# Optimization experiments

Measured on AMD Instinct MI355X. Metric: run time of the kernel, lower is better.

Reference implementation:

```python
import jax, jax.numpy as jnp
import numpy as np
import math

N_EMBD = 2048
N_HEAD = 16
HEAD_DIM = N_EMBD // N_HEAD
EPS = 1e-6

def rms_norm(x, w):
    xf = x.astype(jnp.float32)
    n = xf * jax.lax.rsqrt(jnp.mean(xf * xf, axis=-1, keepdims=True) + EPS)
    return n.astype(x.dtype) * w

def rotate_embeddings(x):
    # pairs (a, b) -> (-b, a), interleaved on last dim
    x2 = x.reshape(*x.shape[:-1], -1, 2)
    rot = jnp.stack([-x2[..., 1], x2[..., 0]], axis=-1)
    return rot.reshape(x.shape)

def rope_angles(T, hd, dtype):
    # pos = 10000 ** ((-2*arange(0, hd, 2) - 1) / hd)  (faithful to source)
    i = jnp.arange(0, hd, 2, dtype=jnp.float32)
    pos = jnp.power(10000.0, (-2.0 * i - 1.0) / hd)
    token_seq = jnp.arange(T, dtype=jnp.float32)[:, None] * pos[None, :]  # [T, hd/2]
    ang = jnp.concatenate([token_seq, token_seq], axis=-1)  # [T, hd]
    return ang.astype(dtype)

def setup_inputs() -> dict:
    key = jax.random.key(0)
    k1, k2, k3 = jax.random.split(key, 3)
    B, T, C = 2, 2048, N_EMBD
    x = jax.random.normal(k1, (B, T, C), dtype=jnp.float32)
    s = 1.0 / math.sqrt(C)
    W_qkv = jax.random.normal(k2, (3 * C, C), dtype=jnp.float32) * s
    W_proj = jax.random.normal(k3, (C, C), dtype=jnp.float32) * s
    g_qk = jnp.ones((C,), dtype=jnp.float32)
    return {"x": x, "W_qkv": W_qkv, "W_proj": W_proj, "g_qk": g_qk}

def reference(x, W_qkv, W_proj, g_qk):
    B, T, C = x.shape
    H, hd = N_HEAD, HEAD_DIM
    qkv = x @ W_qkv.T  # [B, T, 3C]
    q, k, v = jnp.split(qkv, 3, axis=-1)
    q = rms_norm(q, g_qk)
    k = rms_norm(k, g_qk)
    # [B, H, T, hd]
    q = q.reshape(B, T, H, hd).transpose(0, 2, 1, 3)
    k = k.reshape(B, T, H, hd).transpose(0, 2, 1, 3)
    v = v.reshape(B, T, H, hd).transpose(0, 2, 1, 3)
    ang = rope_angles(T, hd, x.dtype)  # [T, hd]
    cos, sin = jnp.cos(ang), jnp.sin(ang)
    q = q * cos + rotate_embeddings(q) * sin
    k = k * cos + rotate_embeddings(k) * sin
    scale = 1.0 / math.sqrt(hd)  # muP = False
    att = jnp.einsum('bhqd,bhkd->bhqk', q, k) * scale
    causal = jnp.tril(jnp.ones((T, T), dtype=bool))
    att = jnp.where(causal, att, -jnp.inf)
    att = jax.nn.softmax(att, axis=-1)
    y = jnp.einsum('bhqk,bhkd->bhqd', att, v)
    y = y.transpose(0, 2, 1, 3).reshape(B, T, C)
    return y @ W_proj.T
```

## Files before the change

### kernel.cpp

```cpp
#include <hip/hip_runtime.h>
#include <math.h>

typedef __bf16 bf16x8 __attribute__((ext_vector_type(8)));
typedef float f32x4 __attribute__((ext_vector_type(4)));

__device__ __forceinline__ unsigned short f2bf(float x) {
  unsigned int u = __builtin_bit_cast(unsigned int, x);
  unsigned int r = (u + 0x7fffu + ((u >> 16) & 1u)) >> 16;
  return (unsigned short)r;
}
__device__ __forceinline__ float bf2f(unsigned short u) {
  return __builtin_bit_cast(float, ((unsigned int)u) << 16);
}
__device__ __forceinline__ void async16(const void* g, void* l) {
  __builtin_amdgcn_global_load_lds(
      (const __attribute__((address_space(1))) void*)g,
      (__attribute__((address_space(3))) void*)l, 16, 0, 0);
}

__global__ __launch_bounds__(256) void cvt_bf16_k(const float* __restrict__ in,
                                                  unsigned short* __restrict__ out,
                                                  int n8) {
  const int i = blockIdx.x * 256 + threadIdx.x;
  if (i >= n8) return;
  const float4* p = (const float4*)in + (long)i * 2;
  const float4 v0 = p[0], v1 = p[1];
  alignas(16) unsigned short o[8] = {f2bf(v0.x), f2bf(v0.y), f2bf(v0.z), f2bf(v0.w),
                                     f2bf(v1.x), f2bf(v1.y), f2bf(v1.z), f2bf(v1.w)};
  *(uint4*)(out + (long)i * 8) = *(uint4*)o;
}

__global__ __launch_bounds__(256) void rope_tab(float2* __restrict__ tab) {
  const int id = blockIdx.x * 256 + threadIdx.x;
  const int t = id >> 6, i = id & 63;
  const float kf = 13.287712379549449f / 128.f;
  const float a = (float)t * exp2f(-(4.f * (float)i + 1.f) * kf);
  float s, c;
  sincosf(a, &s, &c);
  tab[id] = make_float2(c, s);
}

template <int MODE>
__global__ __launch_bounds__(256) void gemm_bf(
    const unsigned short* __restrict__ A, const unsigned short* __restrict__ B,
    void* __restrict__ Cp, unsigned short* __restrict__ Vt, int M, int N, int K) {
  __shared__ unsigned short As[128 * 32];
  __shared__ unsigned short Bs[128 * 32];
  const int tid = threadIdx.x;
  const int lane = tid & 63;
  const int w = tid >> 6;
  const int wr = w >> 1, wc = w & 1;
  const int fr = lane & 15, fq = lane >> 4;
  const long m0 = (long)blockIdx.y * 128;
  const long n0 = (long)blockIdx.x * 128;
  const int sr = lane >> 2, sc = (lane & 3) * 8;
  f32x4 acc[4][4] = {};
  for (int k0 = 0; k0 < K; k0 += 32) {
    __syncthreads();
#pragma unroll
    for (int i = 0; i < 2; i++) {
      const int r = (w * 2 + i) * 16 + sr;
      async16(A + (m0 + r) * (long)K + k0 + sc, &As[(w * 2 + i) * 512]);
      async16(B + (n0 + r) * (long)K + k0 + sc, &Bs[(w * 2 + i) * 512]);
    }
    __syncthreads();
    bf16x8 a[4], b[4];
#pragma unroll
    for (int i = 0; i < 4; i++)
      a[i] = *(const bf16x8*)&As[(wr * 64 + i * 16 + fr) * 32 + fq * 8];
#pragma unroll
    for (int j = 0; j < 4; j++)
      b[j] = *(const bf16x8*)&Bs[(wc * 64 + j * 16 + fr) * 32 + fq * 8];
#pragma unroll
    for (int i = 0; i < 4; i++)
#pragma unroll
      for (int j = 0; j < 4; j++)
        acc[i][j] =
            __builtin_amdgcn_mfma_f32_16x16x32_bf16(a[i], b[j], acc[i][j], 0, 0, 0);
  }
  if (MODE == 0) {
    float* C = (float*)Cp;
#pragma unroll
    for (int i = 0; i < 4; i++)
#pragma unroll
      for (int j = 0; j < 4; j++)
#pragma unroll
        for (int r = 0; r < 4; r++) {
          const long m = m0 + wr * 64 + i * 16 + fq * 4 + r;
          const long n = n0 + wc * 64 + j * 16 + fr;
          C[m * N + n] = acc[i][j][r];
        }
  } else if (n0 < 4096) {
    unsigned short* C = (unsigned short*)Cp;
#pragma unroll
    for (int i = 0; i < 4; i++)
#pragma unroll
      for (int j = 0; j < 4; j++)
#pragma unroll
        for (int r = 0; r < 4; r++) {
          const long m = m0 + wr * 64 + i * 16 + fq * 4 + r;
          const long n = n0 + wc * 64 + j * 16 + fr;
          C[m * 4096 + n] = f2bf(acc[i][j][r]);
        }
  } else {
    const long vb = ((m0 >> 11) * 16 + ((n0 - 4096) >> 7)) * (128L * 2048);
#pragma unroll
    for (int i = 0; i < 4; i++)
#pragma unroll
      for (int j = 0; j < 4; j++) {
        const int d = wc * 64 + j * 16 + fr;
        const int t = (int)(m0 & 2047) + wr * 64 + i * 16 + fq * 4;
        alignas(8) unsigned short o[4] = {f2bf(acc[i][j][0]), f2bf(acc[i][j][1]),
                                          f2bf(acc[i][j][2]), f2bf(acc[i][j][3])};
        *(uint2*)&Vt[vb + (long)d * 2048 + t] = *(uint2*)o;
      }
  }
}

__global__ __launch_bounds__(256) void rms_rope(unsigned short* __restrict__ qkv,
                                                const float* __restrict__ g,
                                                const float2* __restrict__ tab) {
  const int m = blockIdx.x;
  const int t = m & 2047;
  const int tid = threadIdx.x;
  const int lane = tid & 63, w = tid >> 6;
  unsigned short* row = qkv + (long)m * 4096;
  const int base = tid * 8;
  alignas(16) unsigned short qs[8], ks[8];
  *(uint4*)qs = *(const uint4*)(row + base);
  *(uint4*)ks = *(const uint4*)(row + 2048 + base);
  float qv[8], kv[8];
  float sq = 0.f, sk = 0.f;
#pragma unroll
  for (int j = 0; j < 8; j++) {
    qv[j] = bf2f(qs[j]);
    kv[j] = bf2f(ks[j]);
    sq += qv[j] * qv[j];
    sk += kv[j] * kv[j];
  }
#pragma unroll
  for (int off = 1; off < 64; off <<= 1) {
    sq += __shfl_xor(sq, off);
    sk += __shfl_xor(sk, off);
  }
  __shared__ float red[2][4];
  if (lane == 0) {
    red[0][w] = sq;
    red[1][w] = sk;
  }
  __syncthreads();
  sq = red[0][0] + red[0][1] + red[0][2] + red[0][3];
  sk = red[1][0] + red[1][1] + red[1][2] + red[1][3];
  const float rq = rsqrtf(sq * (1.f / 2048.f) + 1e-6f);
  const float rk = rsqrtf(sk * (1.f / 2048.f) + 1e-6f);
  float qn[8], kn[8];
#pragma unroll
  for (int j = 0; j < 8; j++) {
    const float gg = g[base + j];
    qn[j] = qv[j] * rq * gg;
    kn[j] = kv[j] * rk * gg;
  }
  const float2* tp = tab + t * 64 + (base & 63);
  alignas(16) unsigned short qo[8], ko[8];
#pragma unroll
  for (int p = 0; p < 8; p += 2) {
    const float2 cs0 = tp[p];
    const float2 cs1 = tp[p + 1];
    qo[p] = f2bf(qn[p] * cs0.x - qn[p + 1] * cs0.y);
    qo[p + 1] = f2bf(qn[p + 1] * cs1.x + qn[p] * cs1.y);
    ko[p] = f2bf(kn[p] * cs0.x - kn[p + 1] * cs0.y);
    ko[p + 1] = f2bf(kn[p + 1] * cs1.x + kn[p] * cs1.y);
  }
  *(uint4*)(row + base) = *(uint4*)qo;
  *(uint4*)(row + 2048 + base) = *(uint4*)ko;
}

__global__ __launch_bounds__(256, 4) void attn64(
    const unsigned short* __restrict__ QKV, const unsigned short* __restrict__ VT,
    unsigned short* __restrict__ Y) {
  const int qt = (((int)blockIdx.y >> 3) & 1) ? (31 - (int)blockIdx.x)
                                              : (int)blockIdx.x;
  const int bh = blockIdx.y;
  const int b = bh >> 4, h = bh & 15;
  const int tid = threadIdx.x, lane = tid & 63, w = tid >> 6;
  const int fr = lane & 15, fq = lane >> 4;
  __shared__ unsigned short Kl[64 * 136];
  __shared__ unsigned short Vl[128 * 72];
  const long tokbase = (long)b * 2048;
  const unsigned short* Qp = QKV + tokbase * 4096 + h * 128;
  const unsigned short* Kp = Qp + 2048;
  const unsigned short* Vg = VT + (long)bh * (128 * 2048);
  const int qbase = qt * 64;
  bf16x8 aq[4];
  {
    const unsigned short* qp = Qp + (long)(qbase + w * 16 + fr) * 4096 + fq * 8;
#pragma unroll
    for (int ks = 0; ks < 4; ks++) aq[ks] = *(const bf16x8*)(qp + ks * 32);
  }
  float m_i[4], l_i[4];
#pragma unroll
  for (int r = 0; r < 4; r++) {
    m_i[r] = -1e30f;
    l_i[r] = 0.f;
  }
  f32x4 accO[8] = {};
  const int srow = tid >> 4, scol = (tid & 15) * 8;
  const int vrow = tid >> 3, vcol = (tid & 7) * 8;
  for (int kt = 0; kt <= qt; kt++) {
    __syncthreads();
#pragma unroll
    for (int i = 0; i < 4; i++) {
      const int row = i * 16 + srow;
      *(uint4*)&Kl[row * 136 + scol] =
          *(const uint4*)(Kp + (long)(kt * 64 + row) * 4096 + scol);
    }
#pragma unroll
    for (int p = 0; p < 4; p++) {
      const int row = p * 32 + vrow;
      *(uint4*)&Vl[row * 72 + vcol] =
          *(const uint4*)(Vg + (long)row * 2048 + kt * 64 + vcol);
    }
    __syncthreads();
    f32x4 accS[4] = {};
#pragma unroll
    for (int n = 0; n < 4; n++)
#pragma unroll
      for (int ks = 0; ks < 4; ks++) {
        bf16x8 bk = *(const bf16x8*)&Kl[(n * 16 + fr) * 136 + ks * 32 + fq * 8];
        accS[n] = __builtin_amdgcn_mfma_f32_16x16x32_bf16(aq[ks], bk, accS[n], 0, 0, 0);
      }
    const float scale = 0.08838834764831845f;
#pragma unroll
    for (int n = 0; n < 4; n++)
#pragma unroll
      for (int r = 0; r < 4; r++) {
        const float s = accS[n][r] * scale;
        const int key = kt * 64 + n * 16 + fr;
        const int qq = qbase + w * 16 + fq * 4 + r;
        accS[n][r] = (key > qq) ? -1e30f : s;
      }
    float alpha[4];
#pragma unroll
    for (int r = 0; r < 4; r++) {
      float mx = fmaxf(fmaxf(accS[0][r], accS[1][r]), fmaxf(accS[2][r], accS[3][r]));
#pragma unroll
      for (int off = 1; off < 16; off <<= 1) mx = fmaxf(mx, __shfl_xor(mx, off));
      const float mnew = fmaxf(m_i[r], mx);
      alpha[r] = __expf(m_i[r] - mnew);
      m_i[r] = mnew;
    }
#pragma unroll
    for (int n = 0; n < 4; n++)
#pragma unroll
      for (int r = 0; r < 4; r++) accS[n][r] = __expf(accS[n][r] - m_i[r]);
#pragma unroll
    for (int r = 0; r < 4; r++) {
      float sum = accS[0][r] + accS[1][r] + accS[2][r] + accS[3][r];
#pragma unroll
      for (int off = 1; off < 16; off <<= 1) sum += __shfl_xor(sum, off);
      l_i[r] = l_i[r] * alpha[r] + sum;
    }
#pragma unroll
    for (int ds = 0; ds < 8; ds++)
#pragma unroll
      for (int r = 0; r < 4; r++) accO[ds][r] *= alpha[r];
    __syncthreads();
    unsigned short* Pl = Kl + w * 1024;
#pragma unroll
    for (int n = 0; n < 4; n++)
#pragma unroll
      for (int r = 0; r < 4; r++)
        Pl[(fq * 4 + r) * 64 + n * 16 + fr] = f2bf(accS[n][r]);
#pragma unroll
    for (int ks = 0; ks < 2; ks++) {
      bf16x8 ap = *(const bf16x8*)&Pl[fr * 64 + ks * 32 + fq * 8];
#pragma unroll
      for (int ds = 0; ds < 8; ds++) {
        bf16x8 bv = *(const bf16x8*)&Vl[(ds * 16 + fr) * 72 + ks * 32 + fq * 8];
        accO[ds] = __builtin_amdgcn_mfma_f32_16x16x32_bf16(ap, bv, accO[ds], 0, 0, 0);
      }
    }
  }
#pragma unroll
  for (int r = 0; r < 4; r++) l_i[r] = 1.f / l_i[r];
#pragma unroll
  for (int ds = 0; ds < 8; ds++)
#pragma unroll
    for (int r = 0; r < 4; r++) {
      const long trow = tokbase + qbase + w * 16 + fq * 4 + r;
      Y[trow * 2048 + h * 128 + ds * 16 + fr] = f2bf(accO[ds][r] * l_i[r]);
    }
}

extern "C" void kernel_launch(void* const* d_in, const int* in_sizes, int n_in,
                              void* d_out, int out_size, void* d_ws, size_t ws_size,
                              hipStream_t stream) {
  (void)out_size;
  (void)ws_size;
  const float *x = 0, *Wq = 0, *Wp = 0, *g = 0;
  for (int i = 0; i < n_in; i++) {
    switch (in_sizes[i]) {
      case 8388608: x = (const float*)d_in[i]; break;
      case 12582912: Wq = (const float*)d_in[i]; break;
      case 4194304: Wp = (const float*)d_in[i]; break;
      case 2048: g = (const float*)d_in[i]; break;
    }
  }
  if (!x) x = (const float*)d_in[0];
  if (!Wq) Wq = (const float*)d_in[1];
  if (!Wp) Wp = (const float*)d_in[2];
  if (!g) g = (const float*)d_in[3];
  float* out = (float*)d_out;
  char* ws = (char*)d_ws;
  unsigned short* qkv16 = (unsigned short*)ws;
  unsigned short* VtG = (unsigned short*)(ws + 33554432);
  unsigned short* Y = (unsigned short*)(ws + 50331648);
  unsigned short* xb = Y;
  unsigned short* Wqb = (unsigned short*)(ws + 67108864);
  unsigned short* Wpb = (unsigned short*)(ws + 92274688);
  float2* tab = (float2*)(ws + 100663296);

  cvt_bf16_k<<<4096, 256, 0, stream>>>(x, xb, 1048576);
  cvt_bf16_k<<<6144, 256, 0, stream>>>(Wq, Wqb, 1572864);
  cvt_bf16_k<<<2048, 256, 0, stream>>>(Wp, Wpb, 524288);
  rope_tab<<<512, 256, 0, stream>>>(tab);
  gemm_bf<1><<<dim3(48, 32), 256, 0, stream>>>(xb, Wqb, qkv16, VtG, 4096, 6144,
                                               2048);
  rms_rope<<<4096, 256, 0, stream>>>(qkv16, g, tab);
  attn64<<<dim3(32, 32), 256, 0, stream>>>(qkv16, VtG, Y);
  gemm_bf<0><<<dim3(16, 32), 256, 0, stream>>>(Y, Wpb, out, nullptr, 4096, 2048,
                                               2048);
}
```

Measured before the change: 505.8 us.

## Drop LDS staging in attention, add lazy rescale, remap blocks for XCD locality

The attention kernel stops staging K and V tiles in shared memory. Each wave now reads its K and V MFMA operands straight from global memory (relying on cache), which removes the per-tile __syncthreads barriers. Only the P tile stays in LDS, now with an XOR swizzle to avoid bank conflicts. Causal masking is applied only on the diagonal tile, and the running-max rescale of O and l is skipped unless the max grows by more than a threshold. Both the GEMM and attention block indices are remapped so related tiles land on the same XCD for better L2 reuse; the price is redundant global loads per wave that may stress L2 and TLB.

```diff
diff --git a/kernel.cpp b/kernel.cpp
--- a/kernel.cpp
+++ b/kernel.cpp
@@ -51,8 +51,12 @@
   const int w = tid >> 6;
   const int wr = w >> 1, wc = w & 1;
   const int fr = lane & 15, fq = lane >> 4;
-  const long m0 = (long)blockIdx.y * 128;
-  const long n0 = (long)blockIdx.x * 128;
+  const int nbx = gridDim.x;
+  const int nwg = nbx * (int)gridDim.y;
+  int bid = (int)blockIdx.y * nbx + (int)blockIdx.x;
+  bid = (bid & 7) * (nwg >> 3) + (bid >> 3);
+  const long m0 = (long)(bid / nbx) * 128;
+  const long n0 = (long)(bid % nbx) * 128;
   const int sr = lane >> 2, sc = (lane & 3) * 8;
   f32x4 acc[4][4] = {};
   for (int k0 = 0; k0 < K; k0 += 32) {
@@ -178,14 +182,16 @@
 __global__ __launch_bounds__(256, 4) void attn64(
     const unsigned short* __restrict__ QKV, const unsigned short* __restrict__ VT,
     unsigned short* __restrict__ Y) {
-  const int qt = (((int)blockIdx.y >> 3) & 1) ? (31 - (int)blockIdx.x)
-                                              : (int)blockIdx.x;
-  const int bh = blockIdx.y;
+  const int bid = blockIdx.x;
+  const int r_ = bid & 7, s_ = bid >> 3;
+  const int slot = s_ >> 5, j = s_ & 31;
+  const int bh = r_ * 4 + slot;
+  const int qt = (slot & 1) ? (31 - j) : j;
   const int b = bh >> 4, h = bh & 15;
   const int tid = threadIdx.x, lane = tid & 63, w = tid >> 6;
   const int fr = lane & 15, fq = lane >> 4;
-  __shared__ unsigned short Kl[64 * 136];
-  __shared__ unsigned short Vl[128 * 72];
+  __shared__ unsigned short Pl[4][16 * 64];
+  char* Pb = (char*)&Pl[w][0];
   const long tokbase = (long)b * 2048;
   const unsigned short* Qp = QKV + tokbase * 4096 + h * 128;
   const unsigned short* Kp = Qp + 2048;
@@ -204,50 +210,52 @@
     l_i[r] = 0.f;
   }
   f32x4 accO[8] = {};
-  const int srow = tid >> 4, scol = (tid & 15) * 8;
-  const int vrow = tid >> 3, vcol = (tid & 7) * 8;
+  const float scale = 0.08838834764831845f;
   for (int kt = 0; kt <= qt; kt++) {
-    __syncthreads();
-#pragma unroll
-    for (int i = 0; i < 4; i++) {
-      const int row = i * 16 + srow;
-      *(uint4*)&Kl[row * 136 + scol] =
-          *(const uint4*)(Kp + (long)(kt * 64 + row) * 4096 + scol);
-    }
-#pragma unroll
-    for (int p = 0; p < 4; p++) {
-      const int row = p * 32 + vrow;
-      *(uint4*)&Vl[row * 72 + vcol] =
-          *(const uint4*)(Vg + (long)row * 2048 + kt * 64 + vcol);
-    }
-    __syncthreads();
     f32x4 accS[4] = {};
+    const unsigned short* kb = Kp + (long)(kt * 64 + fr) * 4096 + fq * 8;
 #pragma unroll
     for (int n = 0; n < 4; n++)
 #pragma unroll
       for (int ks = 0; ks < 4; ks++) {
-        bf16x8 bk = *(const bf16x8*)&Kl[(n * 16 + fr) * 136 + ks * 32 + fq * 8];
+        bf16x8 bk = *(const bf16x8*)(kb + (long)n * 65536 + ks * 32);
         accS[n] = __builtin_amdgcn_mfma_f32_16x16x32_bf16(aq[ks], bk, accS[n], 0, 0, 0);
       }
-    const float scale = 0.08838834764831845f;
-#pragma unroll
-    for (int n = 0; n < 4; n++)
+    if (kt == qt) {
+#pragma unroll
+      for (int n = 0; n < 4; n++)
+#pragma unroll
+        for (int r = 0; r < 4; r++) {
+          const int key = kt * 64 + n * 16 + fr;
+          const int qq = qbase + w * 16 + fq * 4 + r;
+          accS[n][r] = (key > qq) ? -1e30f : accS[n][r] * scale;
+        }
+    } else {
+#pragma unroll
+      for (int n = 0; n < 4; n++)
+#pragma unroll
+        for (int r = 0; r < 4; r++) accS[n][r] *= scale;
+    }
+    float mx[4];
+    bool need = false;
+#pragma unroll
+    for (int r = 0; r < 4; r++) {
+      float m = fmaxf(fmaxf(accS[0][r], accS[1][r]), fmaxf(accS[2][r], accS[3][r]));
+#pragma unroll
+      for (int off = 1; off < 16; off <<= 1) m = fmaxf(m, __shfl_xor(m, off));
+      mx[r] = m;
+      need |= (m > m_i[r] + 8.f);
+    }
+    if (__any(need)) {
 #pragma unroll
       for (int r = 0; r < 4; r++) {
-        const float s = accS[n][r] * scale;
-        const int key = kt * 64 + n * 16 + fr;
-        const int qq = qbase + w * 16 + fq * 4 + r;
-        accS[n][r] = (key > qq) ? -1e30f : s;
-      }
-    float alpha[4];
-#pragma unroll
-    for (int r = 0; r < 4; r++) {
-      float mx = fmaxf(fmaxf(accS[0][r], accS[1][r]), fmaxf(accS[2][r], accS[3][r]));
-#pragma unroll
-      for (int off = 1; off < 16; off <<= 1) mx = fmaxf(mx, __shfl_xor(mx, off));
-      const float mnew = fmaxf(m_i[r], mx);
-      alpha[r] = __expf(m_i[r] - mnew);
-      m_i[r] = mnew;
+        const float mnew = fmaxf(m_i[r], mx[r]);
+        const float alpha = __expf(m_i[r] - mnew);
+        m_i[r] = mnew;
+        l_i[r] *= alpha;
+#pragma unroll
+        for (int ds = 0; ds < 8; ds++) accO[ds][r] *= alpha;
+      }
     }
 #pragma unroll
     for (int n = 0; n < 4; n++)
@@ -258,25 +266,24 @@
       float sum = accS[0][r] + accS[1][r] + accS[2][r] + accS[3][r];
 #pragma unroll
       for (int off = 1; off < 16; off <<= 1) sum += __shfl_xor(sum, off);
-      l_i[r] = l_i[r] * alpha[r] + sum;
-    }
-#pragma unroll
-    for (int ds = 0; ds < 8; ds++)
-#pragma unroll
-      for (int r = 0; r < 4; r++) accO[ds][r] *= alpha[r];
-    __syncthreads();
-    unsigned short* Pl = Kl + w * 1024;
+      l_i[r] += sum;
+    }
 #pragma unroll
     for (int n = 0; n < 4; n++)
 #pragma unroll
-      for (int r = 0; r < 4; r++)
-        Pl[(fq * 4 + r) * 64 + n * 16 + fr] = f2bf(accS[n][r]);
+      for (int r = 0; r < 4; r++) {
+        const int row = fq * 4 + r;
+        const int byte = row * 128 + ((n * 32 + fr * 2) ^ ((row & 7) << 4));
+        *(unsigned short*)(Pb + byte) = f2bf(accS[n][r]);
+      }
 #pragma unroll
     for (int ks = 0; ks < 2; ks++) {
-      bf16x8 ap = *(const bf16x8*)&Pl[fr * 64 + ks * 32 + fq * 8];
+      bf16x8 ap =
+          *(const bf16x8*)(Pb + fr * 128 + ((ks * 64 + fq * 16) ^ ((fr & 7) << 4)));
 #pragma unroll
       for (int ds = 0; ds < 8; ds++) {
-        bf16x8 bv = *(const bf16x8*)&Vl[(ds * 16 + fr) * 72 + ks * 32 + fq * 8];
+        bf16x8 bv = *(const bf16x8*)(Vg + (long)(ds * 16 + fr) * 2048 + kt * 64 +
+                                     ks * 32 + fq * 8);
         accO[ds] = __builtin_amdgcn_mfma_f32_16x16x32_bf16(ap, bv, accO[ds], 0, 0, 0);
       }
     }
@@ -327,7 +334,7 @@
   gemm_bf<1><<<dim3(48, 32), 256, 0, stream>>>(xb, Wqb, qkv16, VtG, 4096, 6144,
                                                2048);
   rms_rope<<<4096, 256, 0, stream>>>(qkv16, g, tab);
-  attn64<<<dim3(32, 32), 256, 0, stream>>>(qkv16, VtG, Y);
+  attn64<<<1024, 256, 0, stream>>>(qkv16, VtG, Y);
   gemm_bf<0><<<dim3(16, 32), 256, 0, stream>>>(Y, Wpb, out, nullptr, 4096, 2048,
                                                2048);
 }
```

Measured after the change: 636.5 us. 1.26x slower.
